# Kernel tuning notes

Hardware: AMD Instinct MI355X
Metric: run time of the kernel (lower is better)

The kernel has to match this reference:

```python
import math
import jax, jax.numpy as jnp
import numpy as np

B, T, S, C, E = 16, 1024, 1024, 1024, 1024
NORM_C = 0.5


def setup_inputs() -> dict:
    key = jax.random.key(0)
    ks = jax.random.split(key, 9)
    return {
        "x": jax.random.normal(ks[0], (B, T, C), dtype=jnp.float32),
        "target_embedding": jax.random.normal(ks[1], (B, T, E), dtype=jnp.float32),
        "enc_keys": jax.random.normal(ks[2], (B, E, S), dtype=jnp.float32),      # encoder_out[0]
        "enc_values": jax.random.normal(ks[3], (B, S, E), dtype=jnp.float32),    # encoder_out[1]
        "encoder_padding_mask": jax.random.randint(ks[4], (B, S), 0, 2).astype(bool),
        "w_in": jax.random.normal(ks[5], (E, C), dtype=jnp.float32) / np.sqrt(C),
        "b_in": jnp.zeros((E,), dtype=jnp.float32),
        "w_out": jax.random.normal(ks[6], (C, E), dtype=jnp.float32) / np.sqrt(E),
        "b_out": jnp.zeros((C,), dtype=jnp.float32),
    }


def reference(x, target_embedding, enc_keys, enc_values, encoder_padding_mask,
              w_in, b_in, w_out, b_out):
    scale = jnp.float32(math.sqrt(NORM_C))
    residual = x
    # in_projection + target embedding, rescale
    h = (jnp.einsum("btc,ec->bte", x, w_in) + b_in + target_embedding) * scale
    # attention scores: bmm with keys [B,E,S]
    scores = jnp.einsum("bte,bes->bts", h, enc_keys)
    neg_inf = jnp.float32(float("-inf"))
    scores = jnp.where(encoder_padding_mask[:, None, :], neg_inf, scores)
    attn_scores = jax.nn.softmax(scores, axis=-1)
    # weighted sum of values
    ctx = jnp.einsum("bts,bse->bte", attn_scores, enc_values)
    # data-dependent rescale: multiply by sqrt(valid token count)
    s = jnp.float32(S) - jnp.sum(encoder_padding_mask.astype(ctx.dtype), axis=1, keepdims=True)  # [B,1]
    s = s[:, :, None]  # [B,1,1]
    ctx = ctx * (s * jax.lax.rsqrt(s))
    out = (jnp.einsum("bte,ce->btc", ctx, w_out) + b_out + residual) * scale
    return (out, attn_scores)
```

## Files before the change

### kernel.cpp

```cpp
#include <hip/hip_runtime.h>


#define SCALE_F 0.70710678118654752440f

constexpr int BB = 16, TT = 1024, SS = 1024, CC = 1024, EE = 1024;

typedef float    f32x4 __attribute__((ext_vector_type(4)));
typedef _Float16 f16x8 __attribute__((ext_vector_type(8)));
typedef _Float16 f16x4 __attribute__((ext_vector_type(4)));

__device__ __forceinline__ void gload_lds16(const _Float16* g, _Float16* l) {
  __builtin_amdgcn_global_load_lds((const __attribute__((address_space(1))) void*)g,
                                   (__attribute__((address_space(3))) void*)l,
                                   16, 0, 0);
}

#define VMCNT(N) asm volatile("s_waitcnt vmcnt(" #N ")" ::: "memory")
#define LGKM0()  asm volatile("s_waitcnt lgkmcnt(0)" ::: "memory")
#define SBAR()   asm volatile("s_barrier" ::: "memory")

__global__ __launch_bounds__(256) void cvt_f16(const float* __restrict__ s,
                                               _Float16* __restrict__ d, long n) {
  long i = ((long)blockIdx.x * 256 + threadIdx.x) * 8;
  if (i >= n) return;
  f32x4 a = *(const f32x4*)(s + i);
  f32x4 b = *(const f32x4*)(s + i + 4);
  f16x8 h;
  h[0]=(_Float16)a[0]; h[1]=(_Float16)a[1]; h[2]=(_Float16)a[2]; h[3]=(_Float16)a[3];
  h[4]=(_Float16)b[0]; h[5]=(_Float16)b[1]; h[6]=(_Float16)b[2]; h[7]=(_Float16)b[3];
  *(f16x8*)(d + i) = h;
}

__global__ __launch_bounds__(256) void transpose_cvt(const float* __restrict__ src,
                                                     _Float16* __restrict__ dst,
                                                     int R, int Cc) {
  __shared__ float tile[64][65];
  const int b = blockIdx.z;
  const int r0 = blockIdx.y * 64, c0 = blockIdx.x * 64;
  const int t = threadIdx.x;
  const int tr = t >> 4, tc4 = (t & 15) * 4;
  const float* s = src + (size_t)b * R * Cc;
#pragma unroll
  for (int i = 0; i < 4; ++i) {
    f32x4 v = *(const f32x4*)(s + (size_t)(r0 + i * 16 + tr) * Cc + c0 + tc4);
    tile[i * 16 + tr][tc4 + 0] = v[0]; tile[i * 16 + tr][tc4 + 1] = v[1];
    tile[i * 16 + tr][tc4 + 2] = v[2]; tile[i * 16 + tr][tc4 + 3] = v[3];
  }
  __syncthreads();
  _Float16* d = dst + (size_t)b * Cc * R;
#pragma unroll
  for (int j = 0; j < 4; ++j) {
    const int cl = j * 16 + tr;
    f16x4 h;
    h[0] = (_Float16)tile[tc4 + 0][cl]; h[1] = (_Float16)tile[tc4 + 1][cl];
    h[2] = (_Float16)tile[tc4 + 2][cl]; h[3] = (_Float16)tile[tc4 + 3][cl];
    *(f16x4*)(d + (size_t)(c0 + cl) * R + r0 + tc4) = h;
  }
}

__global__ __launch_bounds__(256) void mask_prep(const unsigned char* __restrict__ mraw,
                                                 float* __restrict__ maskneg,
                                                 float* __restrict__ sscale) {
  const int b = blockIdx.x, t = threadIdx.x;
  __shared__ int bytemode_sh, cnt_sh;
  if (t == 0) { bytemode_sh = 0; cnt_sh = 0; }
  __syncthreads();
  const unsigned int* mu = (const unsigned int*)mraw;
  int local = 0;
  for (int i = t; i < (BB * SS) / 4; i += 256) {
    unsigned int v = mu[i];
    if (v != 0u && v != 1u && v != 0x3f800000u) local = 1;
  }
  if (local) atomicOr(&bytemode_sh, 1);
  __syncthreads();
  const int bytemode = bytemode_sh;
  int cnt = 0;
  for (int s = t; s < SS; s += 256) {
    int m = bytemode ? (mraw[b * SS + s] != 0) : (mu[b * SS + s] != 0u);
    maskneg[b * SS + s] = m ? -__builtin_inff() : 0.0f;
    cnt += m;
  }
#pragma unroll
  for (int o = 32; o; o >>= 1) cnt += __shfl_down(cnt, o);
  if ((t & 63) == 0) atomicAdd(&cnt_sh, cnt);
  __syncthreads();
  if (t == 0) {
    float sv = (float)SS - (float)cnt_sh;
    sscale[b] = sv * rsqrtf(sv);
  }
}

template <int EPI>
__global__ __launch_bounds__(512, 2)
void gemm256(const _Float16* __restrict__ A, const _Float16* __restrict__ Bmat,
             long aStride, long bStride, long oStride,
             int M, int N, int K,
             void* __restrict__ outp,
             const float* __restrict__ bias,
             const float* __restrict__ addmat,
             const float* __restrict__ extra) {
  __shared__ __attribute__((aligned(16))) _Float16 smem[73728];

  const int t = threadIdx.x;
  const int lane = t & 63;
  const int wid = t >> 6;
  const int wm = wid >> 1, wn = wid & 1;
  const int z = blockIdx.z;
  const int lo = lane & 15, hi = lane >> 4;
  const int sx = lo & 7;
  const int nt = K >> 6;

  const int gx = gridDim.x;
  const int fblk = blockIdx.x + blockIdx.y * gx;
  const int q = (gx * gridDim.y) >> 3;
  const int wg = (fblk & 7) * q + (fblk >> 3);
  const long rowBase = (long)(wg / gx) * 256;
  const long colBase = (long)(wg % gx) * 128;

  const _Float16* Ag = A + (size_t)z * aStride + rowBase * K;
  const _Float16* Bg = Bmat + (size_t)z * bStride + colBase * K;

  const int srow = t >> 3;
  const int schunk = (t & 7) ^ (srow & 7);
  const int scol = schunk * 8;

  f32x4 acc[4][4] = {};

#define STAGE_A2(U, I0)                                                        \
  {                                                                            \
    _Float16* dst_ = &smem[((U) % 3) * 16384];                                 \
    const long kb_ = (long)(U) * 64 + scol;                                    \
    gload_lds16(Ag + (size_t)((I0)*64 + srow) * K + kb_,                       \
                dst_ + ((I0)*64 + srow) * 64 + (t & 7) * 8);                   \
    gload_lds16(Ag + (size_t)((I0)*64 + 64 + srow) * K + kb_,                  \
                dst_ + ((I0)*64 + 64 + srow) * 64 + (t & 7) * 8);              \
  }
#define STAGE_B1(U, I)                                                         \
  {                                                                            \
    _Float16* dst_ = &smem[49152 + ((U) % 3) * 8192];                          \
    gload_lds16(Bg + (size_t)((I)*64 + srow) * K + (long)(U) * 64 + scol,      \
                dst_ + ((I)*64 + srow) * 64 + (t & 7) * 8);                    \
  }
#define STAGE_TILE(U) STAGE_A2(U, 0) STAGE_A2(U, 2) STAGE_B1(U, 0) STAGE_B1(U, 1)

  STAGE_TILE(0)
  STAGE_TILE(1)
  VMCNT(6);
  SBAR();

  for (int u = 0; u < nt; ++u) {
    const _Float16* As = &smem[(u % 3) * 16384];
    const _Float16* Bs = &smem[49152 + (u % 3) * 8192];
#pragma unroll
    for (int ks = 0; ks < 2; ++ks) {
      f16x8 a[4], b[4];
      const int slot = (ks * 4 + hi) ^ sx;
#pragma unroll
      for (int mi = 0; mi < 4; ++mi)
        a[mi] = *(const f16x8*)&As[(wm * 64 + mi * 16 + lo) * 64 + slot * 8];
#pragma unroll
      for (int ni = 0; ni < 4; ++ni)
        b[ni] = *(const f16x8*)&Bs[(wn * 64 + ni * 16 + lo) * 64 + slot * 8];
      if (u < nt - 2) {
        if (ks == 0) { STAGE_A2(u + 2, 0) STAGE_B1(u + 2, 0) }
        else         { STAGE_A2(u + 2, 2) STAGE_B1(u + 2, 1) }
      }
      LGKM0();
      __builtin_amdgcn_sched_barrier(0);
      __builtin_amdgcn_s_setprio(1);
#pragma unroll
      for (int mi = 0; mi < 4; ++mi)
#pragma unroll
        for (int ni = 0; ni < 4; ++ni)
          acc[mi][ni] = __builtin_amdgcn_mfma_f32_16x16x32_f16(a[mi], b[ni],
                                                               acc[mi][ni], 0, 0, 0);
      __builtin_amdgcn_s_setprio(0);
    }
    if (u < nt - 2)      { VMCNT(6); }
    else if (u == nt - 2){ VMCNT(0); }
    SBAR();
  }

  constexpr int EPS = 68;
  const int fr = lane & 15;
  const int fq = (lane >> 4) * 4;
  const int er = lane >> 2;
  const int ec = (lane & 3) * 16;
  const long gc0 = colBase + wn * 64 + ec;
  float* ep = (float*)smem + wid * (16 * EPS);

  f32x4 biasv[4], maskv[4], av[4];
  float sc = 0.f;
  if constexpr (EPI == 1 || EPI == 4) {
#pragma unroll
    for (int i = 0; i < 4; ++i) biasv[i] = *(const f32x4*)&bias[gc0 + i * 4];
    const long gr0 = rowBase + wm * 64 + er;
#pragma unroll
    for (int i = 0; i < 4; ++i) av[i] = *(const f32x4*)&addmat[gr0 * N + gc0 + i * 4];
  }
  if constexpr (EPI == 2) {
#pragma unroll
    for (int i = 0; i < 4; ++i) maskv[i] = *(const f32x4*)&extra[(size_t)z * N + gc0 + i * 4];
  }
  if constexpr (EPI == 3) sc = extra[z];

#pragma unroll
  for (int mf = 0; mf < 4; ++mf) {
#pragma unroll
    for (int n = 0; n < 4; ++n)
#pragma unroll
      for (int j = 0; j < 4; ++j)
        ep[(fq + j) * EPS + n * 16 + fr] = acc[mf][n][j];
    __syncthreads();
    const long gr = rowBase + wm * 64 + mf * 16 + er;
    f32x4 r[4];
#pragma unroll
    for (int i = 0; i < 4; ++i) r[i] = *(const f32x4*)&ep[er * EPS + ec + i * 4];
    f32x4 a_cur[4];
    if constexpr (EPI == 1 || EPI == 4) {
#pragma unroll
      for (int i = 0; i < 4; ++i) a_cur[i] = av[i];
      if (mf < 3) {
        const long grn = gr + 16;
#pragma unroll
        for (int i = 0; i < 4; ++i) av[i] = *(const f32x4*)&addmat[grn * N + gc0 + i * 4];
      }
    }
    if constexpr (EPI == 1) {
      _Float16* o = (_Float16*)outp + gr * N + gc0;
#pragma unroll
      for (int g = 0; g < 2; ++g) {
        f32x4 v0 = (r[2 * g] + biasv[2 * g] + a_cur[2 * g]) * SCALE_F;
        f32x4 v1 = (r[2 * g + 1] + biasv[2 * g + 1] + a_cur[2 * g + 1]) * SCALE_F;
        f16x8 h;
        h[0]=(_Float16)v0[0]; h[1]=(_Float16)v0[1]; h[2]=(_Float16)v0[2]; h[3]=(_Float16)v0[3];
        h[4]=(_Float16)v1[0]; h[5]=(_Float16)v1[1]; h[6]=(_Float16)v1[2]; h[7]=(_Float16)v1[3];
        *(f16x8*)(o + g * 8) = h;
      }
    } else if constexpr (EPI == 2) {
      float* o = (float*)outp + (size_t)z * oStride + gr * N + gc0;
#pragma unroll
      for (int i = 0; i < 4; ++i) *(f32x4*)(o + i * 4) = r[i] + maskv[i];
    } else if constexpr (EPI == 3) {
      _Float16* o = (_Float16*)outp + (size_t)z * oStride + gr * N + gc0;
#pragma unroll
      for (int g = 0; g < 2; ++g) {
        f32x4 v0 = r[2 * g] * sc;
        f32x4 v1 = r[2 * g + 1] * sc;
        f16x8 h;
        h[0]=(_Float16)v0[0]; h[1]=(_Float16)v0[1]; h[2]=(_Float16)v0[2]; h[3]=(_Float16)v0[3];
        h[4]=(_Float16)v1[0]; h[5]=(_Float16)v1[1]; h[6]=(_Float16)v1[2]; h[7]=(_Float16)v1[3];
        *(f16x8*)(o + g * 8) = h;
      }
    } else {
      float* o = (float*)outp + gr * N + gc0;
#pragma unroll
      for (int i = 0; i < 4; ++i)
        *(f32x4*)(o + i * 4) = (r[i] + biasv[i] + a_cur[i]) * SCALE_F;
    }
    __syncthreads();
  }
}

__global__ __launch_bounds__(256) void softmax_k(float* __restrict__ attn,
                                                 _Float16* __restrict__ attn16) {
  const size_t row = blockIdx.x;
  float* p = attn + row * SS;
  const int t = threadIdx.x;
  f32x4 v = *(const f32x4*)(p + t * 4);
  __shared__ float red[8];
  float m = fmaxf(fmaxf(v[0], v[1]), fmaxf(v[2], v[3]));
#pragma unroll
  for (int o = 32; o; o >>= 1) m = fmaxf(m, __shfl_xor(m, o));
  if (!(t & 63)) red[t >> 6] = m;
  __syncthreads();
  m = fmaxf(fmaxf(red[0], red[1]), fmaxf(red[2], red[3]));
  f32x4 e;
  e[0] = __expf(v[0] - m); e[1] = __expf(v[1] - m);
  e[2] = __expf(v[2] - m); e[3] = __expf(v[3] - m);
  float s = e[0] + e[1] + e[2] + e[3];
#pragma unroll
  for (int o = 32; o; o >>= 1) s += __shfl_xor(s, o);
  if (!(t & 63)) red[4 + (t >> 6)] = s;
  __syncthreads();
  s = red[4] + red[5] + red[6] + red[7];
  const float inv = 1.0f / s;
  f32x4 o4; o4[0]=e[0]*inv; o4[1]=e[1]*inv; o4[2]=e[2]*inv; o4[3]=e[3]*inv;
  *(f32x4*)(p + t * 4) = o4;
  f16x4 h; h[0]=(_Float16)o4[0]; h[1]=(_Float16)o4[1];
  h[2]=(_Float16)o4[2]; h[3]=(_Float16)o4[3];
  *(f16x4*)(attn16 + row * SS + t * 4) = h;
}

extern "C" void kernel_launch(void* const* d_in, const int* in_sizes, int n_in,
                              void* d_out, int out_size, void* d_ws, size_t ws_size,
                              hipStream_t stream) {
  const float* x     = (const float*)d_in[0];
  const float* te    = (const float*)d_in[1];
  const float* keys  = (const float*)d_in[2];
  const float* vals  = (const float*)d_in[3];
  const void*  mask  = d_in[4];
  const float* w_in  = (const float*)d_in[5];
  const float* b_in  = (const float*)d_in[6];
  const float* w_out = (const float*)d_in[7];
  const float* b_out = (const float*)d_in[8];

  char* ws = (char*)d_ws;
  const size_t MB32 = 33554432;
  _Float16* buf0   = (_Float16*)(ws);
  _Float16* buf1   = (_Float16*)(ws + MB32);
  _Float16* keysT  = (_Float16*)(ws + 2 * MB32);
  _Float16* valsT  = (_Float16*)(ws + 3 * MB32);
  _Float16* win16  = (_Float16*)(ws + 4 * MB32);
  _Float16* wout16 = (_Float16*)(ws + 4 * MB32 + 2097152);
  float*    maskneg= (float*)   (ws + 4 * MB32 + 2 * 2097152);
  float*    sscale = (float*)   (ws + 4 * MB32 + 2 * 2097152 + 65536);

  float* out_main = (float*)d_out;
  float* attn_out = (float*)d_out + (size_t)BB * TT * CC;

  cvt_f16<<<dim3(16777216 / 2048), 256, 0, stream>>>(x, buf0, 16777216);
  cvt_f16<<<dim3(1048576 / 2048), 256, 0, stream>>>(w_in, win16, 1048576);
  cvt_f16<<<dim3(1048576 / 2048), 256, 0, stream>>>(w_out, wout16, 1048576);
  transpose_cvt<<<dim3(SS / 64, EE / 64, BB), 256, 0, stream>>>(keys, keysT, EE, SS);
  transpose_cvt<<<dim3(EE / 64, SS / 64, BB), 256, 0, stream>>>(vals, valsT, SS, EE);
  mask_prep<<<dim3(BB), 256, 0, stream>>>((const unsigned char*)mask, maskneg, sscale);

  gemm256<1><<<dim3(EE / 128, (BB * TT) / 256, 1), 512, 0, stream>>>(
      buf0, win16, 0, 0, 0, BB * TT, EE, CC, buf1, b_in, te, nullptr);
  gemm256<2><<<dim3(SS / 128, TT / 256, BB), 512, 0, stream>>>(
      buf1, keysT, (long)TT * EE, (long)SS * EE, (long)TT * SS,
      TT, SS, EE, attn_out, nullptr, nullptr, maskneg);
  softmax_k<<<dim3(BB * TT), 256, 0, stream>>>(attn_out, buf1);
  gemm256<3><<<dim3(EE / 128, TT / 256, BB), 512, 0, stream>>>(
      buf1, valsT, (long)TT * SS, (long)EE * SS, (long)TT * EE,
      TT, EE, SS, buf0, nullptr, nullptr, sscale);
  gemm256<4><<<dim3(CC / 128, (BB * TT) / 256, 1), 512, 0, stream>>>(
      buf0, wout16, 0, 0, 0, BB * TT, CC, EE, out_main, b_out, x, nullptr);
}
```

Before: 330.0 us.

## Enlarge GEMM tile to 256x256 with double-buffered LDS and inline ds_read

```diff
diff --git a/kernel.cpp b/kernel.cpp
--- a/kernel.cpp
+++ b/kernel.cpp
@@ -16,8 +16,10 @@
 }
 
 #define VMCNT(N) asm volatile("s_waitcnt vmcnt(" #N ")" ::: "memory")
-#define LGKM0()  asm volatile("s_waitcnt lgkmcnt(0)" ::: "memory")
+#define LGKM(N)  asm volatile("s_waitcnt lgkmcnt(" #N ")" ::: "memory")
 #define SBAR()   asm volatile("s_barrier" ::: "memory")
+#define DSR(dst, a, off) \
+  asm volatile("ds_read_b128 %0, %1 offset:" #off : "=v"(dst) : "v"(a))
 
 __global__ __launch_bounds__(256) void cvt_f16(const float* __restrict__ s,
                                                _Float16* __restrict__ d, long n) {
@@ -99,12 +101,12 @@
              const float* __restrict__ bias,
              const float* __restrict__ addmat,
              const float* __restrict__ extra) {
-  __shared__ __attribute__((aligned(16))) _Float16 smem[73728];
+  __shared__ __attribute__((aligned(16))) _Float16 smem[65536];
 
   const int t = threadIdx.x;
   const int lane = t & 63;
   const int wid = t >> 6;
-  const int wm = wid >> 1, wn = wid & 1;
+  const int wm = wid >> 2, wn = wid & 3;
   const int z = blockIdx.z;
   const int lo = lane & 15, hi = lane >> 4;
   const int sx = lo & 7;
@@ -115,69 +117,77 @@
   const int q = (gx * gridDim.y) >> 3;
   const int wg = (fblk & 7) * q + (fblk >> 3);
   const long rowBase = (long)(wg / gx) * 256;
-  const long colBase = (long)(wg % gx) * 128;
+  const long colBase = (long)(wg % gx) * 256;
 
   const _Float16* Ag = A + (size_t)z * aStride + rowBase * K;
   const _Float16* Bg = Bmat + (size_t)z * bStride + colBase * K;
 
-  const int srow = t >> 3;
-  const int schunk = (t & 7) ^ (srow & 7);
-  const int scol = schunk * 8;
-
-  f32x4 acc[4][4] = {};
-
-#define STAGE_A2(U, I0)                                                        \
+  const int sr8 = t >> 3;
+  const int srck = (((t & 7) ^ (sr8 & 7)) << 3);
+
+  f32x4 acc[8][4] = {};
+
+#define STAGE8(U)                                                              \
   {                                                                            \
-    _Float16* dst_ = &smem[((U) % 3) * 16384];                                 \
-    const long kb_ = (long)(U) * 64 + scol;                                    \
-    gload_lds16(Ag + (size_t)((I0)*64 + srow) * K + kb_,                       \
-                dst_ + ((I0)*64 + srow) * 64 + (t & 7) * 8);                   \
-    gload_lds16(Ag + (size_t)((I0)*64 + 64 + srow) * K + kb_,                  \
-                dst_ + ((I0)*64 + 64 + srow) * 64 + (t & 7) * 8);              \
-  }
-#define STAGE_B1(U, I)                                                         \
-  {                                                                            \
-    _Float16* dst_ = &smem[49152 + ((U) % 3) * 8192];                          \
-    gload_lds16(Bg + (size_t)((I)*64 + srow) * K + (long)(U) * 64 + scol,      \
-                dst_ + ((I)*64 + srow) * 64 + (t & 7) * 8);                    \
-  }
-#define STAGE_TILE(U) STAGE_A2(U, 0) STAGE_A2(U, 2) STAGE_B1(U, 0) STAGE_B1(U, 1)
-
-  STAGE_TILE(0)
-  STAGE_TILE(1)
-  VMCNT(6);
+    const int tu_ = (U);                                                       \
+    _Float16* db_ = &smem[(tu_ & 1) * 32768];                                  \
+    const size_t kb_ = (size_t)tu_ * 64 + srck;                                \
+    _Pragma("unroll") for (int i_ = 0; i_ < 4; ++i_)                           \
+      gload_lds16(Ag + (size_t)(i_ * 64 + sr8) * K + kb_,                      \
+                  db_ + i_ * 4096 + t * 8);                                    \
+    _Pragma("unroll") for (int i_ = 0; i_ < 4; ++i_)                           \
+      gload_lds16(Bg + (size_t)(i_ * 64 + sr8) * K + kb_,                      \
+                  db_ + 16384 + i_ * 4096 + t * 8);                            \
+  }
+
+  const int lds0 = (int)(size_t)&smem[0];
+  const int abase = lds0 + (wm * 128 + lo) * 128 + ((hi ^ sx) << 4);
+  const int bbase = lds0 + 32768 + (wn * 64 + lo) * 128 + ((hi ^ sx) << 4);
+
+  STAGE8(0)
+  STAGE8(1)
+  VMCNT(8);
   SBAR();
 
   for (int u = 0; u < nt; ++u) {
-    const _Float16* As = &smem[(u % 3) * 16384];
-    const _Float16* Bs = &smem[49152 + (u % 3) * 8192];
-#pragma unroll
-    for (int ks = 0; ks < 2; ++ks) {
-      f16x8 a[4], b[4];
-      const int slot = (ks * 4 + hi) ^ sx;
-#pragma unroll
-      for (int mi = 0; mi < 4; ++mi)
-        a[mi] = *(const f16x8*)&As[(wm * 64 + mi * 16 + lo) * 64 + slot * 8];
+    const int bo = (u & 1) << 16;
+    const int aad = abase + bo, bad = bbase + bo;
+    const int aad1 = aad ^ 64, bad1 = bad ^ 64;
+    f16x8 a0[8], b0[4], a1[8], b1[4];
+    DSR(a0[0], aad, 0);     DSR(a0[1], aad, 2048);  DSR(a0[2], aad, 4096);
+    DSR(a0[3], aad, 6144);  DSR(a0[4], aad, 8192);  DSR(a0[5], aad, 10240);
+    DSR(a0[6], aad, 12288); DSR(a0[7], aad, 14336);
+    DSR(b0[0], bad, 0);     DSR(b0[1], bad, 2048);  DSR(b0[2], bad, 4096);
+    DSR(b0[3], bad, 6144);
+    DSR(a1[0], aad1, 0);     DSR(a1[1], aad1, 2048);  DSR(a1[2], aad1, 4096);
+    DSR(a1[3], aad1, 6144);  DSR(a1[4], aad1, 8192);  DSR(a1[5], aad1, 10240);
+    DSR(a1[6], aad1, 12288); DSR(a1[7], aad1, 14336);
+    DSR(b1[0], bad1, 0);     DSR(b1[1], bad1, 2048);  DSR(b1[2], bad1, 4096);
+    DSR(b1[3], bad1, 6144);
+    LGKM(12);
+    __builtin_amdgcn_sched_barrier(0);
+    __builtin_amdgcn_s_setprio(1);
+#pragma unroll
+    for (int mi = 0; mi < 8; ++mi)
 #pragma unroll
       for (int ni = 0; ni < 4; ++ni)
-        b[ni] = *(const f16x8*)&Bs[(wn * 64 + ni * 16 + lo) * 64 + slot * 8];
-      if (u < nt - 2) {
-        if (ks == 0) { STAGE_A2(u + 2, 0) STAGE_B1(u + 2, 0) }
-        else         { STAGE_A2(u + 2, 2) STAGE_B1(u + 2, 1) }
-      }
-      LGKM0();
-      __builtin_amdgcn_sched_barrier(0);
-      __builtin_amdgcn_s_setprio(1);
-#pragma unroll
-      for (int mi = 0; mi < 4; ++mi)
-#pragma unroll
-        for (int ni = 0; ni < 4; ++ni)
-          acc[mi][ni] = __builtin_amdgcn_mfma_f32_16x16x32_f16(a[mi], b[ni],
-                                                               acc[mi][ni], 0, 0, 0);
-      __builtin_amdgcn_s_setprio(0);
-    }
-    if (u < nt - 2)      { VMCNT(6); }
-    else if (u == nt - 2){ VMCNT(0); }
+        acc[mi][ni] = __builtin_amdgcn_mfma_f32_16x16x32_f16(a0[mi], b0[ni],
+                                                             acc[mi][ni], 0, 0, 0);
+    __builtin_amdgcn_s_setprio(0);
+    LGKM(0);
+    __builtin_amdgcn_sched_barrier(0);
+    SBAR();
+    if (u + 2 < nt) STAGE8(u + 2)
+    __builtin_amdgcn_s_setprio(1);
+#pragma unroll
+    for (int mi = 0; mi < 8; ++mi)
+#pragma unroll
+      for (int ni = 0; ni < 4; ++ni)
+        acc[mi][ni] = __builtin_amdgcn_mfma_f32_16x16x32_f16(a1[mi], b1[ni],
+                                                             acc[mi][ni], 0, 0, 0);
+    __builtin_amdgcn_s_setprio(0);
+    if (u + 2 < nt)       { VMCNT(8); }
+    else if (u + 2 == nt) { VMCNT(0); }
     SBAR();
   }
 
@@ -194,7 +204,7 @@
   if constexpr (EPI == 1 || EPI == 4) {
 #pragma unroll
     for (int i = 0; i < 4; ++i) biasv[i] = *(const f32x4*)&bias[gc0 + i * 4];
-    const long gr0 = rowBase + wm * 64 + er;
+    const long gr0 = rowBase + wm * 128 + er;
 #pragma unroll
     for (int i = 0; i < 4; ++i) av[i] = *(const f32x4*)&addmat[gr0 * N + gc0 + i * 4];
   }
@@ -204,15 +214,16 @@
   }
   if constexpr (EPI == 3) sc = extra[z];
 
-#pragma unroll
-  for (int mf = 0; mf < 4; ++mf) {
+  __syncthreads();
+#pragma unroll
+  for (int mf = 0; mf < 8; ++mf) {
 #pragma unroll
     for (int n = 0; n < 4; ++n)
 #pragma unroll
       for (int j = 0; j < 4; ++j)
         ep[(fq + j) * EPS + n * 16 + fr] = acc[mf][n][j];
     __syncthreads();
-    const long gr = rowBase + wm * 64 + mf * 16 + er;
+    const long gr = rowBase + wm * 128 + mf * 16 + er;
     f32x4 r[4];
 #pragma unroll
     for (int i = 0; i < 4; ++i) r[i] = *(const f32x4*)&ep[er * EPS + ec + i * 4];
@@ -220,7 +231,7 @@
     if constexpr (EPI == 1 || EPI == 4) {
 #pragma unroll
       for (int i = 0; i < 4; ++i) a_cur[i] = av[i];
-      if (mf < 3) {
+      if (mf < 7) {
         const long grn = gr + 16;
 #pragma unroll
         for (int i = 0; i < 4; ++i) av[i] = *(const f32x4*)&addmat[grn * N + gc0 + i * 4];
@@ -326,15 +337,15 @@
   transpose_cvt<<<dim3(EE / 64, SS / 64, BB), 256, 0, stream>>>(vals, valsT, SS, EE);
   mask_prep<<<dim3(BB), 256, 0, stream>>>((const unsigned char*)mask, maskneg, sscale);
 
-  gemm256<1><<<dim3(EE / 128, (BB * TT) / 256, 1), 512, 0, stream>>>(
+  gemm256<1><<<dim3(EE / 256, (BB * TT) / 256, 1), 512, 0, stream>>>(
       buf0, win16, 0, 0, 0, BB * TT, EE, CC, buf1, b_in, te, nullptr);
-  gemm256<2><<<dim3(SS / 128, TT / 256, BB), 512, 0, stream>>>(
+  gemm256<2><<<dim3(SS / 256, TT / 256, BB), 512, 0, stream>>>(
       buf1, keysT, (long)TT * EE, (long)SS * EE, (long)TT * SS,
       TT, SS, EE, attn_out, nullptr, nullptr, maskneg);
   softmax_k<<<dim3(BB * TT), 256, 0, stream>>>(attn_out, buf1);
-  gemm256<3><<<dim3(EE / 128, TT / 256, BB), 512, 0, stream>>>(
+  gemm256<3><<<dim3(EE / 256, TT / 256, BB), 512, 0, stream>>>(
       buf1, valsT, (long)TT * SS, (long)EE * SS, (long)TT * EE,
       TT, EE, SS, buf0, nullptr, nullptr, sscale);
-  gemm256<4><<<dim3(CC / 128, (BB * TT) / 256, 1), 512, 0, stream>>>(
+  gemm256<4><<<dim3(CC / 256, (BB * TT) / 256, 1), 512, 0, stream>>>(
       buf0, wout16, 0, 0, 0, BB * TT, CC, EE, out_main, b_out, x, nullptr);
 }
```

After: 314.8 us. 1.05x faster.
